# Kernel optimization log

Measured on AMD Instinct MI355X. Metric: run time of the kernel, lower is better.

Reference implementation:

```python
import jax, jax.numpy as jnp
import numpy as np

EDGE_DIM = 128
HIDDEN = 128
E = 200000
G = 500000
LN_EPS = 1e-5


def _layer_norm(x, gamma, beta):
    mu = jnp.mean(x, axis=-1, keepdims=True)
    var = jnp.mean(jnp.square(x - mu), axis=-1, keepdims=True)
    return (x - mu) * jax.lax.rsqrt(var + LN_EPS) * gamma + beta


def setup_inputs() -> dict:
    key = jax.random.key(0)
    ks = jax.random.split(key, 12)
    d2 = EDGE_DIM * 2          # 256
    h2 = HIDDEN * 2            # 256
    s1 = 1.0 / np.sqrt(d2)
    s2 = 1.0 / np.sqrt(h2)
    s3 = 1.0 / np.sqrt(HIDDEN + 1)
    return {
        "edge_embeddings": jax.random.normal(ks[0], (E, EDGE_DIM), dtype=jnp.float32),
        "edge_groups": jax.random.randint(ks[1], (G, 2), 0, E, dtype=jnp.int32),
        "importance_scores": jax.random.uniform(ks[2], (G,), dtype=jnp.float32),
        # group_mlp: Linear(d2 -> h2), GELU, LayerNorm(h2), Linear(h2 -> H), ReLU, LayerNorm(H)
        "W1": jax.random.uniform(ks[3], (d2, h2), jnp.float32, -s1, s1),
        "b1": jax.random.uniform(ks[4], (h2,), jnp.float32, -s1, s1),
        "g1": jnp.ones((h2,), jnp.float32),
        "be1": jnp.zeros((h2,), jnp.float32),
        "W2": jax.random.uniform(ks[5], (h2, HIDDEN), jnp.float32, -s2, s2),
        "b2": jax.random.uniform(ks[6], (HIDDEN,), jnp.float32, -s2, s2),
        "g2": jnp.ones((HIDDEN,), jnp.float32),
        "be2": jnp.zeros((HIDDEN,), jnp.float32),
        # importance_modulation: Linear(H+1 -> H), ReLU
        "Wm": jax.random.uniform(ks[7], (HIDDEN + 1, HIDDEN), jnp.float32, -s3, s3),
        "bm": jax.random.uniform(ks[8], (HIDDEN,), jnp.float32, -s3, s3),
    }


def reference(edge_embeddings, edge_groups, importance_scores,
              W1, b1, g1, be1, W2, b2, g2, be2, Wm, bm):
    # Batched gather of both edge endpoints: [G, edge_dim] each
    emb_i = edge_embeddings[edge_groups[:, 0]]
    emb_j = edge_embeddings[edge_groups[:, 1]]
    concat_emb = jnp.concatenate([emb_i, emb_j], axis=-1)  # [G, 2*edge_dim]
    # group_mlp(concat_emb)  (the attention/weighted branch in the source is dead code)
    h = jax.nn.gelu(concat_emb @ W1 + b1, approximate=False)
    h = _layer_norm(h, g1, be1)
    h = jax.nn.relu(h @ W2 + b2)
    group_emb = _layer_norm(h, g2, be2)                    # [G, hidden]
    # importance modulation
    x = jnp.concatenate([group_emb, importance_scores[:, None]], axis=-1)  # [G, hidden+1]
    return jax.nn.relu(x @ Wm + bm)                        # [G, hidden]
```

## Files before the change

kernel.cpp:

```cpp
#include <hip/hip_runtime.h>

typedef __attribute__((ext_vector_type(8))) short s16x8;
typedef __attribute__((ext_vector_type(4))) float f32x4;

#define LN_EPS 1e-5f

__device__ __forceinline__ unsigned short f2bf(float f) {
  unsigned int u = __float_as_uint(f);
  u += 0x7fffu + ((u >> 16) & 1u);
  return (unsigned short)(u >> 16);
}

__device__ __forceinline__ unsigned cvt_pk_bf16(float lo, float hi) {
  unsigned r;
  asm("v_cvt_pk_bf16_f32 %0, %1, %2" : "=v"(r) : "v"(lo), "v"(hi));
  return r;
}

__device__ __forceinline__ float gelu_fast(float x) {
  float x2 = x * x;
  float y = x * (0.7978845608f + 0.03567740814f * x2);
  float t = __expf(-2.0f * fabsf(y));
  float th = (1.0f - t) / (1.0f + t);
  th = copysignf(th, y);
  return 0.5f * x * (1.0f + th);
}

__global__ void prep_weights(const float* __restrict__ W1, const float* __restrict__ W2,
                             const float* __restrict__ Wm, unsigned short* __restrict__ ws) {
  int i = blockIdx.x * 256 + threadIdx.x;
  if (i < 65536) {
    int f = i >> 9, lane = (i >> 3) & 63, j = i & 7;
    int w = f >> 4, kk = (f >> 1) & 7, nf = f & 1;
    int n = w * 32 + nf * 16 + (lane & 15);
    int k = kk * 32 + (lane >> 4) * 8 + j;
    ws[i] = f2bf(W1[k * 256 + n]);
  } else if (i < 98304) {
    int t = i - 65536;
    int f = t >> 9, lane = (t >> 3) & 63, j = t & 7;
    int w = f >> 3, kk = f & 7;
    int n = w * 16 + (lane & 15);
    int k = kk * 32 + (lane >> 4) * 8 + j;
    ws[i] = f2bf(W2[k * 128 + n]);
  } else if (i < 114688) {
    int t = i - 98304;
    int f = t >> 9, lane = (t >> 3) & 63, j = t & 7;
    int w = f >> 2, kk = f & 3;
    int n = w * 16 + (lane & 15);
    int k = kk * 32 + (lane >> 4) * 8 + j;
    ws[i] = f2bf(Wm[k * 128 + n]);
  } else if (i < 114944) {
    int c = i - 114688;
    reinterpret_cast<float*>(ws + 114688)[c] = Wm[128 * 128 + c];
  }
}

__global__ __launch_bounds__(512, 2) void fused_edge_group(
    const float* __restrict__ emb, const int* __restrict__ eg,
    const float* __restrict__ imp,
    const float* __restrict__ b1, const float* __restrict__ g1, const float* __restrict__ be1,
    const float* __restrict__ b2, const float* __restrict__ g2, const float* __restrict__ be2,
    const float* __restrict__ bm,
    const unsigned short* __restrict__ ws,
    float* __restrict__ out, int G) {

  __shared__ __align__(16) char sh[64 * 520];
  __shared__ float st[2][8][64];
  __shared__ float murs[2][64];

  const int tid = threadIdx.x;
  const int lane = tid & 63;
  const int w = tid >> 6;
  const int l15 = lane & 15;
  const int lgrp = lane >> 4;
  const int g0 = blockIdx.x * 64;

  #pragma unroll
  for (int it = 0; it < 4; ++it) {
    int s = tid + it * 512;
    int row = s >> 5, sc = s & 31;
    int g = g0 + row; if (g >= G) g = G - 1;
    int idx = eg[2 * g + (sc >> 4)];
    const float4* p = reinterpret_cast<const float4*>(emb + (size_t)idx * 128 + (sc & 15) * 8);
    float4 va = p[0], vb = p[1];
    uint4 v;
    v.x = cvt_pk_bf16(va.x, va.y); v.y = cvt_pk_bf16(va.z, va.w);
    v.z = cvt_pk_bf16(vb.x, vb.y); v.w = cvt_pk_bf16(vb.z, vb.w);
    *reinterpret_cast<uint4*>(sh + row * 520 + sc * 16) = v;
  }
  __syncthreads();

  f32x4 acc[4][2];
  #pragma unroll
  for (int mt = 0; mt < 4; ++mt) {
    acc[mt][0] = (f32x4){0.f, 0.f, 0.f, 0.f};
    acc[mt][1] = (f32x4){0.f, 0.f, 0.f, 0.f};
  }
  {
    const unsigned short* ws1w = ws + w * 8192;
    s16x8 wA[2][2];
    wA[0][0] = *reinterpret_cast<const s16x8*>(ws1w + 0 * 512 + lane * 8);
    wA[0][1] = *reinterpret_cast<const s16x8*>(ws1w + 1 * 512 + lane * 8);
    #pragma unroll
    for (int kk = 0; kk < 8; ++kk) {
      if (kk < 7) {
        wA[(kk + 1) & 1][0] = *reinterpret_cast<const s16x8*>(ws1w + ((kk + 1) * 2 + 0) * 512 + lane * 8);
        wA[(kk + 1) & 1][1] = *reinterpret_cast<const s16x8*>(ws1w + ((kk + 1) * 2 + 1) * 512 + lane * 8);
      }
      #pragma unroll
      for (int mt = 0; mt < 4; ++mt) {
        s16x8 xf = *reinterpret_cast<const s16x8*>(sh + (mt * 16 + l15) * 520 + kk * 64 + lgrp * 16);
        acc[mt][0] = __builtin_amdgcn_mfma_f32_16x16x32_bf16(wA[kk & 1][0], xf, acc[mt][0], 0, 0, 0);
        acc[mt][1] = __builtin_amdgcn_mfma_f32_16x16x32_bf16(wA[kk & 1][1], xf, acc[mt][1], 0, 0, 0);
      }
    }
  }

  {
    float4 b1v0 = *reinterpret_cast<const float4*>(b1 + w * 32 + lgrp * 4);
    float4 b1v1 = *reinterpret_cast<const float4*>(b1 + w * 32 + 16 + lgrp * 4);
    #pragma unroll
    for (int mt = 0; mt < 4; ++mt) {
      float s = 0.f, q = 0.f;
      #pragma unroll
      for (int r = 0; r < 4; ++r) {
        float x0 = gelu_fast(acc[mt][0][r] + ((const float*)&b1v0)[r]);
        float x1 = gelu_fast(acc[mt][1][r] + ((const float*)&b1v1)[r]);
        acc[mt][0][r] = x0; acc[mt][1][r] = x1;
        s += x0 + x1; q += x0 * x0 + x1 * x1;
      }
      s += __shfl_xor(s, 16); q += __shfl_xor(q, 16);
      s += __shfl_xor(s, 32); q += __shfl_xor(q, 32);
      if (lane < 16) { st[0][w][mt * 16 + lane] = s; st[1][w][mt * 16 + lane] = q; }
    }
  }
  __syncthreads();
  if (tid < 64) {
    float ms = 0.f, mq = 0.f;
    #pragma unroll
    for (int w2 = 0; w2 < 8; ++w2) { ms += st[0][w2][tid]; mq += st[1][w2][tid]; }
    float mu = ms * (1.f / 256.f);
    float var = mq * (1.f / 256.f) - mu * mu;
    murs[0][tid] = mu; murs[1][tid] = rsqrtf(var + LN_EPS);
  }
  __syncthreads();
  {
    float4 g1v0 = *reinterpret_cast<const float4*>(g1 + w * 32 + lgrp * 4);
    float4 g1v1 = *reinterpret_cast<const float4*>(g1 + w * 32 + 16 + lgrp * 4);
    float4 be1v0 = *reinterpret_cast<const float4*>(be1 + w * 32 + lgrp * 4);
    float4 be1v1 = *reinterpret_cast<const float4*>(be1 + w * 32 + 16 + lgrp * 4);
    #pragma unroll
    for (int mt = 0; mt < 4; ++mt) {
      int row = mt * 16 + l15;
      float mu = murs[0][row], rs = murs[1][row];
      float y[8];
      #pragma unroll
      for (int r = 0; r < 4; ++r) {
        y[r]     = fmaf((acc[mt][0][r] - mu) * rs, ((const float*)&g1v0)[r], ((const float*)&be1v0)[r]);
        y[4 + r] = fmaf((acc[mt][1][r] - mu) * rs, ((const float*)&g1v1)[r], ((const float*)&be1v1)[r]);
      }
      uint2 p0, p1;
      p0.x = cvt_pk_bf16(y[0], y[1]); p0.y = cvt_pk_bf16(y[2], y[3]);
      p1.x = cvt_pk_bf16(y[4], y[5]); p1.y = cvt_pk_bf16(y[6], y[7]);
      char* rp = sh + row * 520 + (w * 32 + lgrp * 4) * 2;
      *reinterpret_cast<uint2*>(rp) = p0;
      *reinterpret_cast<uint2*>(rp + 32) = p1;
    }
  }
  __syncthreads();

  f32x4 acc2[4];
  #pragma unroll
  for (int mt = 0; mt < 4; ++mt) acc2[mt] = (f32x4){0.f, 0.f, 0.f, 0.f};
  {
    const unsigned short* ws2w = ws + 65536 + w * 4096;
    s16x8 wA[2];
    wA[0] = *reinterpret_cast<const s16x8*>(ws2w + lane * 8);
    #pragma unroll
    for (int kk = 0; kk < 8; ++kk) {
      if (kk < 7)
        wA[(kk + 1) & 1] = *reinterpret_cast<const s16x8*>(ws2w + (kk + 1) * 512 + lane * 8);
      #pragma unroll
      for (int mt = 0; mt < 4; ++mt) {
        s16x8 xf = *reinterpret_cast<const s16x8*>(sh + (mt * 16 + l15) * 520 + kk * 64 + lgrp * 16);
        acc2[mt] = __builtin_amdgcn_mfma_f32_16x16x32_bf16(wA[kk & 1], xf, acc2[mt], 0, 0, 0);
      }
    }
  }

  {
    float4 b2v = *reinterpret_cast<const float4*>(b2 + w * 16 + lgrp * 4);
    #pragma unroll
    for (int mt = 0; mt < 4; ++mt) {
      float s = 0.f, q = 0.f;
      #pragma unroll
      for (int r = 0; r < 4; ++r) {
        float x = fmaxf(acc2[mt][r] + ((const float*)&b2v)[r], 0.f);
        acc2[mt][r] = x;
        s += x; q += x * x;
      }
      s += __shfl_xor(s, 16); q += __shfl_xor(q, 16);
      s += __shfl_xor(s, 32); q += __shfl_xor(q, 32);
      if (lane < 16) { st[0][w][mt * 16 + lane] = s; st[1][w][mt * 16 + lane] = q; }
    }
  }
  __syncthreads();
  if (tid < 64) {
    float ms = 0.f, mq = 0.f;
    #pragma unroll
    for (int w2 = 0; w2 < 8; ++w2) { ms += st[0][w2][tid]; mq += st[1][w2][tid]; }
    float mu = ms * (1.f / 128.f);
    float var = mq * (1.f / 128.f) - mu * mu;
    murs[0][tid] = mu; murs[1][tid] = rsqrtf(var + LN_EPS);
  }
  __syncthreads();
  {
    float4 g2v = *reinterpret_cast<const float4*>(g2 + w * 16 + lgrp * 4);
    float4 be2v = *reinterpret_cast<const float4*>(be2 + w * 16 + lgrp * 4);
    #pragma unroll
    for (int mt = 0; mt < 4; ++mt) {
      int row = mt * 16 + l15;
      float mu = murs[0][row], rs = murs[1][row];
      float y[4];
      #pragma unroll
      for (int r = 0; r < 4; ++r)
        y[r] = fmaf((acc2[mt][r] - mu) * rs, ((const float*)&g2v)[r], ((const float*)&be2v)[r]);
      uint2 p;
      p.x = cvt_pk_bf16(y[0], y[1]); p.y = cvt_pk_bf16(y[2], y[3]);
      *reinterpret_cast<uint2*>(sh + row * 264 + (w * 16 + lgrp * 4) * 2) = p;
    }
  }
  __syncthreads();

  f32x4 acc3[4];
  #pragma unroll
  for (int mt = 0; mt < 4; ++mt) acc3[mt] = (f32x4){0.f, 0.f, 0.f, 0.f};
  {
    const unsigned short* ws3w = ws + 98304 + w * 2048;
    s16x8 wA[2];
    wA[0] = *reinterpret_cast<const s16x8*>(ws3w + lane * 8);
    #pragma unroll
    for (int kk = 0; kk < 4; ++kk) {
      if (kk < 3)
        wA[(kk + 1) & 1] = *reinterpret_cast<const s16x8*>(ws3w + (kk + 1) * 512 + lane * 8);
      #pragma unroll
      for (int mt = 0; mt < 4; ++mt) {
        s16x8 xf = *reinterpret_cast<const s16x8*>(sh + (mt * 16 + l15) * 264 + kk * 64 + lgrp * 16);
        acc3[mt] = __builtin_amdgcn_mfma_f32_16x16x32_bf16(wA[kk & 1], xf, acc3[mt], 0, 0, 0);
      }
    }
  }

  {
    int col0 = w * 16 + lgrp * 4;
    float4 bmv = *reinterpret_cast<const float4*>(bm + col0);
    float4 wlv = *reinterpret_cast<const float4*>(reinterpret_cast<const float*>(ws + 114688) + col0);
    #pragma unroll
    for (int mt = 0; mt < 4; ++mt) {
      int g = g0 + mt * 16 + l15;
      float impv = imp[g < G ? g : (G - 1)];
      float4 y;
      y.x = fmaxf(acc3[mt][0] + bmv.x + impv * wlv.x, 0.f);
      y.y = fmaxf(acc3[mt][1] + bmv.y + impv * wlv.y, 0.f);
      y.z = fmaxf(acc3[mt][2] + bmv.z + impv * wlv.z, 0.f);
      y.w = fmaxf(acc3[mt][3] + bmv.w + impv * wlv.w, 0.f);
      if (g < G)
        *reinterpret_cast<float4*>(out + (size_t)g * 128 + col0) = y;
    }
  }
}

extern "C" void kernel_launch(void* const* d_in, const int* in_sizes, int n_in,
                              void* d_out, int out_size, void* d_ws, size_t ws_size,
                              hipStream_t stream) {
  const float* emb = (const float*)d_in[0];
  const int* eg    = (const int*)d_in[1];
  const float* imp = (const float*)d_in[2];
  const float* W1  = (const float*)d_in[3];
  const float* b1  = (const float*)d_in[4];
  const float* g1  = (const float*)d_in[5];
  const float* be1 = (const float*)d_in[6];
  const float* W2  = (const float*)d_in[7];
  const float* b2  = (const float*)d_in[8];
  const float* g2  = (const float*)d_in[9];
  const float* be2 = (const float*)d_in[10];
  const float* Wm  = (const float*)d_in[11];
  const float* bm  = (const float*)d_in[12];
  unsigned short* ws = (unsigned short*)d_ws;
  float* out = (float*)d_out;
  int G = in_sizes[2];

  prep_weights<<<(114944 + 255) / 256, 256, 0, stream>>>(W1, W2, Wm, ws);
  int nblk = (G + 63) / 64;
  fused_edge_group<<<nblk, 512, 0, stream>>>(emb, eg, imp, b1, g1, be1, b2, g2, be2, bm,
                                             ws, out, G);
}
```

Baseline: 250.4 us.

## Remove LayerNorm reduction barriers, prefetch next-layer weights, raise MFMA priority

Each LayerNorm now has every thread sum the eight per-wave partial sums for its row straight from a transposed shared-memory layout. This replaces the single-wave finalize step and drops one __syncthreads per LayerNorm. The first weight fragment of each GEMM is now loaded before the preceding epilogue (and layer 1's before the gather), so the global load latency is hidden. s_setprio raises wave priority around the MFMA loops. The cost is redundant reduction work per thread and extra registers held across phases.

```diff
diff --git a/kernel.cpp b/kernel.cpp
--- a/kernel.cpp
+++ b/kernel.cpp
@@ -65,8 +65,7 @@
     float* __restrict__ out, int G) {
 
   __shared__ __align__(16) char sh[64 * 520];
-  __shared__ float st[2][8][64];
-  __shared__ float murs[2][64];
+  __shared__ __align__(16) float st[64][2][8];
 
   const int tid = threadIdx.x;
   const int lane = tid & 63;
@@ -74,6 +73,14 @@
   const int l15 = lane & 15;
   const int lgrp = lane >> 4;
   const int g0 = blockIdx.x * 64;
+
+  const unsigned short* ws1w = ws + w * 8192;
+  const unsigned short* ws2w = ws + 65536 + w * 4096;
+  const unsigned short* ws3w = ws + 98304 + w * 2048;
+
+  s16x8 wA[2][2];
+  wA[0][0] = *reinterpret_cast<const s16x8*>(ws1w + 0 * 512 + lane * 8);
+  wA[0][1] = *reinterpret_cast<const s16x8*>(ws1w + 1 * 512 + lane * 8);
 
   #pragma unroll
   for (int it = 0; it < 4; ++it) {
@@ -96,25 +103,23 @@
     acc[mt][0] = (f32x4){0.f, 0.f, 0.f, 0.f};
     acc[mt][1] = (f32x4){0.f, 0.f, 0.f, 0.f};
   }
-  {
-    const unsigned short* ws1w = ws + w * 8192;
-    s16x8 wA[2][2];
-    wA[0][0] = *reinterpret_cast<const s16x8*>(ws1w + 0 * 512 + lane * 8);
-    wA[0][1] = *reinterpret_cast<const s16x8*>(ws1w + 1 * 512 + lane * 8);
-    #pragma unroll
-    for (int kk = 0; kk < 8; ++kk) {
-      if (kk < 7) {
-        wA[(kk + 1) & 1][0] = *reinterpret_cast<const s16x8*>(ws1w + ((kk + 1) * 2 + 0) * 512 + lane * 8);
-        wA[(kk + 1) & 1][1] = *reinterpret_cast<const s16x8*>(ws1w + ((kk + 1) * 2 + 1) * 512 + lane * 8);
-      }
-      #pragma unroll
-      for (int mt = 0; mt < 4; ++mt) {
-        s16x8 xf = *reinterpret_cast<const s16x8*>(sh + (mt * 16 + l15) * 520 + kk * 64 + lgrp * 16);
-        acc[mt][0] = __builtin_amdgcn_mfma_f32_16x16x32_bf16(wA[kk & 1][0], xf, acc[mt][0], 0, 0, 0);
-        acc[mt][1] = __builtin_amdgcn_mfma_f32_16x16x32_bf16(wA[kk & 1][1], xf, acc[mt][1], 0, 0, 0);
-      }
-    }
-  }
+  __builtin_amdgcn_s_setprio(1);
+  #pragma unroll
+  for (int kk = 0; kk < 8; ++kk) {
+    if (kk < 7) {
+      wA[(kk + 1) & 1][0] = *reinterpret_cast<const s16x8*>(ws1w + ((kk + 1) * 2 + 0) * 512 + lane * 8);
+      wA[(kk + 1) & 1][1] = *reinterpret_cast<const s16x8*>(ws1w + ((kk + 1) * 2 + 1) * 512 + lane * 8);
+    }
+    #pragma unroll
+    for (int mt = 0; mt < 4; ++mt) {
+      s16x8 xf = *reinterpret_cast<const s16x8*>(sh + (mt * 16 + l15) * 520 + kk * 64 + lgrp * 16);
+      acc[mt][0] = __builtin_amdgcn_mfma_f32_16x16x32_bf16(wA[kk & 1][0], xf, acc[mt][0], 0, 0, 0);
+      acc[mt][1] = __builtin_amdgcn_mfma_f32_16x16x32_bf16(wA[kk & 1][1], xf, acc[mt][1], 0, 0, 0);
+    }
+  }
+  __builtin_amdgcn_s_setprio(0);
+
+  s16x8 w2p = *reinterpret_cast<const s16x8*>(ws2w + lane * 8);
 
   {
     float4 b1v0 = *reinterpret_cast<const float4*>(b1 + w * 32 + lgrp * 4);
@@ -131,17 +136,8 @@
       }
       s += __shfl_xor(s, 16); q += __shfl_xor(q, 16);
       s += __shfl_xor(s, 32); q += __shfl_xor(q, 32);
-      if (lane < 16) { st[0][w][mt * 16 + lane] = s; st[1][w][mt * 16 + lane] = q; }
-    }
-  }
-  __syncthreads();
-  if (tid < 64) {
-    float ms = 0.f, mq = 0.f;
-    #pragma unroll
-    for (int w2 = 0; w2 < 8; ++w2) { ms += st[0][w2][tid]; mq += st[1][w2][tid]; }
-    float mu = ms * (1.f / 256.f);
-    float var = mq * (1.f / 256.f) - mu * mu;
-    murs[0][tid] = mu; murs[1][tid] = rsqrtf(var + LN_EPS);
+      if (lane < 16) { st[mt * 16 + lane][0][w] = s; st[mt * 16 + lane][1][w] = q; }
+    }
   }
   __syncthreads();
   {
@@ -152,7 +148,12 @@
     #pragma unroll
     for (int mt = 0; mt < 4; ++mt) {
       int row = mt * 16 + l15;
-      float mu = murs[0][row], rs = murs[1][row];
+      const float4* sp = reinterpret_cast<const float4*>(&st[row][0][0]);
+      float4 sa = sp[0], sb = sp[1], qa = sp[2], qb = sp[3];
+      float ssum = (sa.x + sa.y) + (sa.z + sa.w) + (sb.x + sb.y) + (sb.z + sb.w);
+      float qsum = (qa.x + qa.y) + (qa.z + qa.w) + (qb.x + qb.y) + (qb.z + qb.w);
+      float mu = ssum * (1.f / 256.f);
+      float rs = rsqrtf(qsum * (1.f / 256.f) - mu * mu + LN_EPS);
       float y[8];
       #pragma unroll
       for (int r = 0; r < 4; ++r) {
@@ -173,20 +174,23 @@
   #pragma unroll
   for (int mt = 0; mt < 4; ++mt) acc2[mt] = (f32x4){0.f, 0.f, 0.f, 0.f};
   {
-    const unsigned short* ws2w = ws + 65536 + w * 4096;
-    s16x8 wA[2];
-    wA[0] = *reinterpret_cast<const s16x8*>(ws2w + lane * 8);
+    s16x8 wB[2];
+    wB[0] = w2p;
+    __builtin_amdgcn_s_setprio(1);
     #pragma unroll
     for (int kk = 0; kk < 8; ++kk) {
       if (kk < 7)
-        wA[(kk + 1) & 1] = *reinterpret_cast<const s16x8*>(ws2w + (kk + 1) * 512 + lane * 8);
+        wB[(kk + 1) & 1] = *reinterpret_cast<const s16x8*>(ws2w + (kk + 1) * 512 + lane * 8);
       #pragma unroll
       for (int mt = 0; mt < 4; ++mt) {
         s16x8 xf = *reinterpret_cast<const s16x8*>(sh + (mt * 16 + l15) * 520 + kk * 64 + lgrp * 16);
-        acc2[mt] = __builtin_amdgcn_mfma_f32_16x16x32_bf16(wA[kk & 1], xf, acc2[mt], 0, 0, 0);
-      }
-    }
-  }
+        acc2[mt] = __builtin_amdgcn_mfma_f32_16x16x32_bf16(wB[kk & 1], xf, acc2[mt], 0, 0, 0);
+      }
+    }
+    __builtin_amdgcn_s_setprio(0);
+  }
+
+  s16x8 w3p = *reinterpret_cast<const s16x8*>(ws3w + lane * 8);
 
   {
     float4 b2v = *reinterpret_cast<const float4*>(b2 + w * 16 + lgrp * 4);
@@ -201,17 +205,8 @@
       }
       s += __shfl_xor(s, 16); q += __shfl_xor(q, 16);
       s += __shfl_xor(s, 32); q += __shfl_xor(q, 32);
-      if (lane < 16) { st[0][w][mt * 16 + lane] = s; st[1][w][mt * 16 + lane] = q; }
-    }
-  }
-  __syncthreads();
-  if (tid < 64) {
-    float ms = 0.f, mq = 0.f;
-    #pragma unroll
-    for (int w2 = 0; w2 < 8; ++w2) { ms += st[0][w2][tid]; mq += st[1][w2][tid]; }
-    float mu = ms * (1.f / 128.f);
-    float var = mq * (1.f / 128.f) - mu * mu;
-    murs[0][tid] = mu; murs[1][tid] = rsqrtf(var + LN_EPS);
+      if (lane < 16) { st[mt * 16 + lane][0][w] = s; st[mt * 16 + lane][1][w] = q; }
+    }
   }
   __syncthreads();
   {
@@ -220,7 +215,12 @@
     #pragma unroll
     for (int mt = 0; mt < 4; ++mt) {
       int row = mt * 16 + l15;
-      float mu = murs[0][row], rs = murs[1][row];
+      const float4* sp = reinterpret_cast<const float4*>(&st[row][0][0]);
+      float4 sa = sp[0], sb = sp[1], qa = sp[2], qb = sp[3];
+      float ssum = (sa.x + sa.y) + (sa.z + sa.w) + (sb.x + sb.y) + (sb.z + sb.w);
+      float qsum = (qa.x + qa.y) + (qa.z + qa.w) + (qb.x + qb.y) + (qb.z + qb.w);
+      float mu = ssum * (1.f / 128.f);
+      float rs = rsqrtf(qsum * (1.f / 128.f) - mu * mu + LN_EPS);
       float y[4];
       #pragma unroll
       for (int r = 0; r < 4; ++r)
@@ -236,19 +236,20 @@
   #pragma unroll
   for (int mt = 0; mt < 4; ++mt) acc3[mt] = (f32x4){0.f, 0.f, 0.f, 0.f};
   {
-    const unsigned short* ws3w = ws + 98304 + w * 2048;
-    s16x8 wA[2];
-    wA[0] = *reinterpret_cast<const s16x8*>(ws3w + lane * 8);
+    s16x8 wC[2];
+    wC[0] = w3p;
+    __builtin_amdgcn_s_setprio(1);
     #pragma unroll
     for (int kk = 0; kk < 4; ++kk) {
       if (kk < 3)
-        wA[(kk + 1) & 1] = *reinterpret_cast<const s16x8*>(ws3w + (kk + 1) * 512 + lane * 8);
+        wC[(kk + 1) & 1] = *reinterpret_cast<const s16x8*>(ws3w + (kk + 1) * 512 + lane * 8);
       #pragma unroll
       for (int mt = 0; mt < 4; ++mt) {
         s16x8 xf = *reinterpret_cast<const s16x8*>(sh + (mt * 16 + l15) * 264 + kk * 64 + lgrp * 16);
-        acc3[mt] = __builtin_amdgcn_mfma_f32_16x16x32_bf16(wA[kk & 1], xf, acc3[mt], 0, 0, 0);
-      }
-    }
+        acc3[mt] = __builtin_amdgcn_mfma_f32_16x16x32_bf16(wC[kk & 1], xf, acc3[mt], 0, 0, 0);
+      }
+    }
+    __builtin_amdgcn_s_setprio(0);
   }
 
   {
```

After: 278.9 us. +11.4%, slower.
